# Kernel tuning notes

Hardware: AMD Instinct MI355X
Metric: run time of the kernel (lower is better)

## Reference

```python
import jax, jax.numpy as jnp
import numpy as np

KS = (7, 7)
ST = (3, 3)
PD = (3, 3)
DIM = 512
HID = 1960  # 40 * 49, divisible by kernel_shape


def _patch_flat_idx(out_h, out_w):
    kh, kw = KS; sh, sw = ST; ph, pw = PD
    oh = (out_h + 2 * ph - kh) // sh + 1
    ow = (out_w + 2 * pw - kw) // sw + 1
    Wp = out_w + 2 * pw
    iy = jnp.arange(kh)[:, None, None, None] + (jnp.arange(oh) * sh)[None, None, :, None]
    ix = jnp.arange(kw)[None, :, None, None] + (jnp.arange(ow) * sw)[None, None, None, :]
    # (kh, kw, oh, ow) flat index into padded image
    return (iy * Wp + ix), oh, ow


def fold(patches, out_h, out_w):
    # patches: (B, C*kh*kw, L) -> (B, C, out_h, out_w), overlap-add like F.fold
    kh, kw = KS; ph, pw = PD
    idx, oh, ow = _patch_flat_idx(out_h, out_w)
    B, CK, L = patches.shape
    C = CK // (kh * kw)
    Hp, Wp = out_h + 2 * ph, out_w + 2 * pw
    p = patches.reshape(B, C, kh, kw, oh, ow)
    out = jnp.zeros((B, C, Hp * Wp), patches.dtype)
    out = out.at[:, :, idx.reshape(-1)].add(p.reshape(B, C, -1))
    return out.reshape(B, C, Hp, Wp)[:, :, ph:ph + out_h, pw:pw + out_w]


def unfold(img, out_h, out_w):
    # img: (B, C, H, W) -> (B, C*kh*kw, L), like F.unfold
    kh, kw = KS; ph, pw = PD
    idx, oh, ow = _patch_flat_idx(out_h, out_w)
    B, C = img.shape[:2]
    imgp = jnp.pad(img, ((0, 0), (0, 0), (ph, ph), (pw, pw)))
    flat = imgp.reshape(B, C, -1)
    g = flat[:, :, idx.reshape(-1)].reshape(B, C, kh, kw, oh, ow)
    return g.reshape(B, C * kh * kw, oh * ow)


def setup_inputs() -> dict:
    key = jax.random.key(0)
    k1, k2, k3, k4, k5 = jax.random.split(key, 5)
    x = jax.random.normal(k1, (2, 5760, DIM), dtype=jnp.float32)
    W1 = jax.random.normal(k2, (HID, DIM), dtype=jnp.float32) * 0.02
    b1 = jax.random.normal(k3, (HID,), dtype=jnp.float32) * 0.02
    W2 = jax.random.normal(k4, (DIM, HID), dtype=jnp.float32) * 0.02
    b2 = jax.random.normal(k5, (DIM,), dtype=jnp.float32) * 0.02
    return {"x": x, "W1": W1, "b1": b1, "W2": W2, "b2": b2, "out_h": 60, "out_w": 108}


def reference(x, W1, b1, W2, b2, out_h, out_w):
    kh, kw = KS; sh, sw = ST; ph, pw = PD
    oh = (out_h + 2 * ph - kh) // sh + 1
    ow = (out_w + 2 * pw - kw) // sw + 1
    n_vecs = oh * ow
    h = jnp.einsum('bnd,hd->bnh', x, W1) + b1          # (b, n, HID)
    b_, n, c = h.shape
    p = h.reshape(-1, n_vecs, c).transpose(0, 2, 1)     # (B', c, L)
    folded = fold(p, out_h, out_w)                      # (B', c//49, H, W)
    ones = jnp.ones((p.shape[0], kh * kw, n_vecs), h.dtype)
    norm = fold(ones, out_h, out_w)                     # (B', 1, H, W)
    y = unfold(folded / norm, out_h, out_w)             # (B', c, L)
    y = y.transpose(0, 2, 1).reshape(b_, n, c)
    out = jnp.einsum('bnh,dh->bnd', jax.nn.gelu(y, approximate=False), W2) + b2
    return out
```

## Files before the change

### kernel.cpp

```cpp
#include <hip/hip_runtime.h>
#include <cmath>

#define M_ROWS   11520
#define DIM      512
#define HID      1960
#define HIDP     2048
#define KP2      1984
#define OH       20
#define OW       36
#define LVEC     720
#define NCH      40
#define BPRIME   16
#define HP       66
#define WP       114

typedef unsigned short u16;
typedef __bf16 bf16x8 __attribute__((ext_vector_type(8)));
typedef float  f32x4  __attribute__((ext_vector_type(4)));

__device__ __forceinline__ u16 f2bf(float f) {
    unsigned u = __float_as_uint(f);
    u += 0x7fffu + ((u >> 16) & 1u);
    return (u16)(u >> 16);
}
__device__ __forceinline__ float bf2f(u16 h) {
    return __uint_as_float(((unsigned)h) << 16);
}

__device__ __forceinline__ void gload_lds16(const void* g, void* l) {
    __builtin_amdgcn_global_load_lds(
        (const __attribute__((address_space(1))) void*)g,
        (__attribute__((address_space(3))) void*)l, 16, 0, 0);
}

__global__ __launch_bounds__(256) void cvt_x(const float* __restrict__ src,
                                             u16* __restrict__ dst, int n) {
    int i = (blockIdx.x * 256 + threadIdx.x) * 4;
    if (i < n) {
        float4 v = *(const float4*)(src + i);
        ushort4 o;
        o.x = f2bf(v.x); o.y = f2bf(v.y); o.z = f2bf(v.z); o.w = f2bf(v.w);
        *(ushort4*)(dst + i) = o;
    }
}

__global__ __launch_bounds__(256) void cvt_w1(const float* __restrict__ src,
                                              u16* __restrict__ dst) {
    int i = (blockIdx.x * 256 + threadIdx.x) * 4;
    ushort4 o;
    if (i < HID * DIM) {
        float4 v = *(const float4*)(src + i);
        o.x = f2bf(v.x); o.y = f2bf(v.y); o.z = f2bf(v.z); o.w = f2bf(v.w);
    } else {
        o.x = o.y = o.z = o.w = 0;
    }
    *(ushort4*)(dst + i) = o;
}

__global__ __launch_bounds__(256) void cvt_w2(const float* __restrict__ src,
                                              u16* __restrict__ dst) {
    int i = (blockIdx.x * 256 + threadIdx.x) * 4;
    int d = i / HIDP, c = i % HIDP;
    ushort4 o;
    if (c < HID) {
        float4 v = *(const float4*)(src + d * HID + c);
        o.x = f2bf(v.x); o.y = f2bf(v.y); o.z = f2bf(v.z); o.w = f2bf(v.w);
    } else {
        o.x = o.y = o.z = o.w = 0;
    }
    *(ushort4*)(dst + i) = o;
}

template <int OUT_BF16, int BN>
__global__ __launch_bounds__(256) void gemm_bt(const u16* __restrict__ A,
                                               const u16* __restrict__ B,
                                               const float* __restrict__ bias,
                                               int biasN, void* __restrict__ Cout,
                                               int N, int K, int ldk) {
    constexpr int WN = BN / 2;
    constexpr int NU = WN / 16;

    __shared__ u16 sA[128 * 64];
    __shared__ u16 sB[BN * 64];

    const int tid  = threadIdx.x;
    const int ntn  = N / BN;
    const int NB   = gridDim.x;
    const int v    = (blockIdx.x & 7) * (NB >> 3) + (blockIdx.x >> 3);
    const int bm   = v / ntn;
    const int bn   = v - bm * ntn;
    const int lane = tid & 63;
    const int wv   = tid >> 6;
    const int wm   = (wv >> 1) * 64;
    const int wn   = (wv & 1) * WN;
    const int r    = lane & 15;
    const int quad = lane >> 4;

    const size_t Arow0 = (size_t)bm * 128 * ldk;
    const size_t Brow0 = (size_t)bn * BN * ldk;

    f32x4 acc[4][NU] = {};

    for (int kt = 0; kt < K; kt += 64) {
        __syncthreads();
#pragma unroll
        for (int i = 0; i < 4; i++) {
            int e   = i * 256 + tid;
            int row = e >> 3;
            int cp  = e & 7;
            int cg  = cp ^ (row & 7);
            gload_lds16(A + Arow0 + (size_t)row * ldk + kt + cg * 8, (char*)sA + e * 16);
        }
#pragma unroll
        for (int i = 0; i < (BN * 8) / 256; i++) {
            int e   = i * 256 + tid;
            int row = e >> 3;
            int cp  = e & 7;
            int cg  = cp ^ (row & 7);
            gload_lds16(B + Brow0 + (size_t)row * ldk + kt + cg * 8, (char*)sB + e * 16);
        }
        __syncthreads();
#pragma unroll
        for (int kk = 0; kk < 2; kk++) {
            bf16x8 af[4], bg[NU];
#pragma unroll
            for (int t = 0; t < 4; t++) {
                int row = wm + t * 16 + r;
                int c   = (kk * 4 + quad) ^ (row & 7);
                af[t] = *(const bf16x8*)(sA + row * 64 + c * 8);
            }
#pragma unroll
            for (int u = 0; u < NU; u++) {
                int row = wn + u * 16 + r;
                int c   = (kk * 4 + quad) ^ (row & 7);
                bg[u] = *(const bf16x8*)(sB + row * 64 + c * 8);
            }
#pragma unroll
            for (int t = 0; t < 4; t++)
#pragma unroll
                for (int u = 0; u < NU; u++)
                    acc[t][u] = __builtin_amdgcn_mfma_f32_16x16x32_bf16(
                        af[t], bg[u], acc[t][u], 0, 0, 0);
        }
    }

    const int gm0 = bm * 128 + wm;
    const int gn0 = bn * BN + wn;
#pragma unroll
    for (int u = 0; u < NU; u++) {
        int gn = gn0 + u * 16 + r;
        float bv = (gn < biasN) ? bias[gn] : 0.0f;
#pragma unroll
        for (int t = 0; t < 4; t++) {
            int gm = gm0 + t * 16 + quad * 4;
#pragma unroll
            for (int q = 0; q < 4; q++) {
                float v2 = acc[t][u][q] + bv;
                if (OUT_BF16)
                    ((u16*)Cout)[(size_t)(gm + q) * N + gn] = f2bf(v2);
                else
                    ((float*)Cout)[(size_t)(gm + q) * N + gn] = v2;
            }
        }
    }
}

__global__ __launch_bounds__(256) void midA_fold(const u16* __restrict__ hg,
                                                 u16* __restrict__ G) {
    __shared__ u16 sh[7 * OW * 49];

    const int b  = blockIdx.x;
    const int bp = b / (NCH * 4);
    const int rr = b - bp * (NCH * 4);
    const int ch = rr >> 2;
    const int s  = rr & 3;
    const int lo    = (s == 0) ? 0 : (5 * s - 2);
    const int nload = (s == 0) ? 5 : 7;
    const int row0  = 15 * s;
    const int nrows = (s == 3) ? 21 : 15;
    const int n0 = bp * LVEC;
    const int c0 = ch * 49;
    const int tid = threadIdx.x;

    for (int i = tid; i < nload * OW * 49; i += 256) {
        int l = i / 49, k = i - l * 49;
        sh[i] = hg[(size_t)(n0 + lo * OW + l) * HIDP + c0 + k];
    }
    __syncthreads();

    const int px = tid & 127;
    const int rg = tid >> 7;
    if (px >= WP) return;

    const bool pxin = (px >= 3) && (px <= 110);
    const int kx0 = px % 3;
    int  ct[3];
    bool vx[3];
    int  cx = 0;
#pragma unroll
    for (int dx = 0; dx < 3; dx++) {
        int kx = kx0 + 3 * dx, rx = px - kx;
        bool ok = pxin && (kx <= 6) && (rx >= 0) && (rx <= 105);
        vx[dx] = ok;
        ct[dx] = ok ? ((rx / 3) * 49 + kx) : 0;
        cx += ok ? 1 : 0;
    }
    const float fcx = (cx == 3) ? (1.0f / 3.0f) : ((cx == 2) ? 0.5f : 1.0f);

    u16* Gb = G + (size_t)(bp * NCH + ch) * (HP * WP);
    for (int ri = rg; ri < nrows; ri += 2) {
        int py = row0 + ri;
        float val = 0.0f;
        if (pxin && py >= 3 && py <= 62) {
            int ky0 = py % 3;
            float sum = 0.0f;
            int cy = 0;
#pragma unroll
            for (int dy = 0; dy < 3; dy++) {
                int ky = ky0 + 3 * dy, ry = py - ky;
                if (ky <= 6 && ry >= 0 && ry <= 57) {
                    int rt = (ry / 3 - lo) * (OW * 49) + ky * 7;
                    cy++;
                    float v0 = bf2f(sh[rt + ct[0]]);
                    float v1 = bf2f(sh[rt + ct[1]]);
                    float v2 = bf2f(sh[rt + ct[2]]);
                    sum += vx[0] ? v0 : 0.0f;
                    sum += vx[1] ? v1 : 0.0f;
                    sum += vx[2] ? v2 : 0.0f;
                }
            }
            float fcy = (cy == 3) ? (1.0f / 3.0f) : ((cy == 2) ? 0.5f : 1.0f);
            float m = sum * fcx * fcy;
            val = 0.5f * m * (1.0f + erff(m * 0.70710678118654752f));
        }
        Gb[py * WP + px] = f2bf(val);
    }
}

__global__ __launch_bounds__(256) void midB_unfold(const u16* __restrict__ G,
                                                   u16* __restrict__ hg) {
    __shared__ u16 sG[34 * WP];

    const int b  = blockIdx.x;
    const int bp = b / (NCH * 2);
    const int rr = b - bp * (NCH * 2);
    const int ch = rr >> 1;
    const int s  = rr & 1;
    const int o0 = s * 10;
    const int n0 = bp * LVEC + o0 * OW;
    const int c0 = ch * 49;
    const int tid = threadIdx.x;

    const u16* Gb = G + (size_t)(bp * NCH + ch) * (HP * WP) + 3 * o0 * WP;
    for (int p = tid; p < 34 * WP; p += 256) sG[p] = Gb[p];
    __syncthreads();

    for (int i = tid; i < 10 * OW * 49; i += 256) {
        int l = i / 49, k = i - l * 49;
        int ky = k / 7, kx = k - ky * 7;
        int oy = l / OW, ox = l - oy * OW;
        hg[(size_t)(n0 + l) * HIDP + c0 + k] = sG[(3 * oy + ky) * WP + kx + 3 * ox];
    }
}

extern "C" void kernel_launch(void* const* d_in, const int* in_sizes, int n_in,
                              void* d_out, int out_size, void* d_ws, size_t ws_size,
                              hipStream_t stream) {
    (void)in_sizes; (void)n_in; (void)out_size; (void)ws_size;
    const float* x  = (const float*)d_in[0];
    const float* W1 = (const float*)d_in[1];
    const float* b1 = (const float*)d_in[2];
    const float* W2 = (const float*)d_in[3];
    const float* b2 = (const float*)d_in[4];
    float* out = (float*)d_out;

    char* ws = (char*)d_ws;
    u16* xb  = (u16*)(ws);
    u16* W1b = (u16*)(ws + 11796480);
    u16* W2b = (u16*)(ws + 11796480 + 2097152);
    u16* hg  = (u16*)(ws + 11796480 + 2097152 + 2097152);
    u16* G   = xb;

    cvt_x <<<(M_ROWS * DIM) / (256 * 4), 256, 0, stream>>>(x, xb, M_ROWS * DIM);
    cvt_w1<<<(HIDP * DIM) / (256 * 4), 256, 0, stream>>>(W1, W1b);
    cvt_w2<<<(DIM * HIDP) / (256 * 4), 256, 0, stream>>>(W2, W2b);

    gemm_bt<1, 128><<<(M_ROWS / 128) * (HIDP / 128), 256, 0, stream>>>(
        xb, W1b, b1, HID, (void*)hg, HIDP, DIM, DIM);

    midA_fold<<<BPRIME * NCH * 4, 256, 0, stream>>>(hg, G);
    midB_unfold<<<BPRIME * NCH * 2, 256, 0, stream>>>(G, hg);

    gemm_bt<0, 64><<<(M_ROWS / 128) * (DIM / 64), 256, 0, stream>>>(
        hg, W2b, b2, DIM, (void*)out, DIM, KP2, HIDP);
}
```

Measured before the change: 209.5 us.

## Merge conversion kernels and run GEMMs with 512-thread blocks of 8 waves

Folds the three fp32-to-bf16 conversion kernels into one launch that picks its source by block index, saving two kernel launches. The GEMM now uses 512 threads, so each of 8 waves computes a 32-row slice instead of 64 rows with 4 waves. This halves per-wave accumulators and raises the number of waves sharing each LDS tile, trading register pressure for more latency hiding. Each wave now issues fewer MFMAs per LDS fragment load, which raises LDS traffic relative to compute.

```diff
diff --git a/kernel.cpp b/kernel.cpp
--- a/kernel.cpp
+++ b/kernel.cpp
@@ -33,52 +33,53 @@
         (__attribute__((address_space(3))) void*)l, 16, 0, 0);
 }
 
-__global__ __launch_bounds__(256) void cvt_x(const float* __restrict__ src,
-                                             u16* __restrict__ dst, int n) {
-    int i = (blockIdx.x * 256 + threadIdx.x) * 4;
-    if (i < n) {
-        float4 v = *(const float4*)(src + i);
-        ushort4 o;
+#define CVT_XB   5760
+#define CVT_W1B  1024
+__global__ __launch_bounds__(256) void cvt_all(const float* __restrict__ x,
+                                               const float* __restrict__ W1,
+                                               const float* __restrict__ W2,
+                                               u16* __restrict__ xb,
+                                               u16* __restrict__ W1b,
+                                               u16* __restrict__ W2b) {
+    const int b = blockIdx.x;
+    const int tid = threadIdx.x;
+    ushort4 o;
+    if (b < CVT_XB) {
+        int i = (b * 256 + tid) * 4;
+        float4 v = *(const float4*)(x + i);
         o.x = f2bf(v.x); o.y = f2bf(v.y); o.z = f2bf(v.z); o.w = f2bf(v.w);
-        *(ushort4*)(dst + i) = o;
-    }
-}
-
-__global__ __launch_bounds__(256) void cvt_w1(const float* __restrict__ src,
-                                              u16* __restrict__ dst) {
-    int i = (blockIdx.x * 256 + threadIdx.x) * 4;
-    ushort4 o;
-    if (i < HID * DIM) {
-        float4 v = *(const float4*)(src + i);
-        o.x = f2bf(v.x); o.y = f2bf(v.y); o.z = f2bf(v.z); o.w = f2bf(v.w);
+        *(ushort4*)(xb + i) = o;
+    } else if (b < CVT_XB + CVT_W1B) {
+        int i = ((b - CVT_XB) * 256 + tid) * 4;
+        if (i < HID * DIM) {
+            float4 v = *(const float4*)(W1 + i);
+            o.x = f2bf(v.x); o.y = f2bf(v.y); o.z = f2bf(v.z); o.w = f2bf(v.w);
+        } else {
+            o.x = o.y = o.z = o.w = 0;
+        }
+        *(ushort4*)(W1b + i) = o;
     } else {
-        o.x = o.y = o.z = o.w = 0;
-    }
-    *(ushort4*)(dst + i) = o;
-}
-
-__global__ __launch_bounds__(256) void cvt_w2(const float* __restrict__ src,
-                                              u16* __restrict__ dst) {
-    int i = (blockIdx.x * 256 + threadIdx.x) * 4;
-    int d = i / HIDP, c = i % HIDP;
-    ushort4 o;
-    if (c < HID) {
-        float4 v = *(const float4*)(src + d * HID + c);
-        o.x = f2bf(v.x); o.y = f2bf(v.y); o.z = f2bf(v.z); o.w = f2bf(v.w);
-    } else {
-        o.x = o.y = o.z = o.w = 0;
-    }
-    *(ushort4*)(dst + i) = o;
+        int i = ((b - CVT_XB - CVT_W1B) * 256 + tid) * 4;
+        int d = i / HIDP, c = i - d * HIDP;
+        if (c < HID) {
+            float4 v = *(const float4*)(W2 + (size_t)d * HID + c);
+            o.x = f2bf(v.x); o.y = f2bf(v.y); o.z = f2bf(v.z); o.w = f2bf(v.w);
+        } else {
+            o.x = o.y = o.z = o.w = 0;
+        }
+        *(ushort4*)(W2b + i) = o;
+    }
 }
 
 template <int OUT_BF16, int BN>
-__global__ __launch_bounds__(256) void gemm_bt(const u16* __restrict__ A,
+__global__ __launch_bounds__(512) void gemm_bt(const u16* __restrict__ A,
                                                const u16* __restrict__ B,
                                                const float* __restrict__ bias,
                                                int biasN, void* __restrict__ Cout,
                                                int N, int K, int ldk) {
     constexpr int WN = BN / 2;
     constexpr int NU = WN / 16;
+    constexpr int BCH = BN * 8;
 
     __shared__ u16 sA[128 * 64];
     __shared__ u16 sB[BN * 64];
@@ -91,7 +92,7 @@
     const int bn   = v - bm * ntn;
     const int lane = tid & 63;
     const int wv   = tid >> 6;
-    const int wm   = (wv >> 1) * 64;
+    const int wm   = (wv >> 1) * 32;
     const int wn   = (wv & 1) * WN;
     const int r    = lane & 15;
     const int quad = lane >> 4;
@@ -99,21 +100,21 @@
     const size_t Arow0 = (size_t)bm * 128 * ldk;
     const size_t Brow0 = (size_t)bn * BN * ldk;
 
-    f32x4 acc[4][NU] = {};
+    f32x4 acc[2][NU] = {};
 
     for (int kt = 0; kt < K; kt += 64) {
         __syncthreads();
 #pragma unroll
-        for (int i = 0; i < 4; i++) {
-            int e   = i * 256 + tid;
+        for (int i = 0; i < 2; i++) {
+            int e   = i * 512 + tid;
             int row = e >> 3;
             int cp  = e & 7;
             int cg  = cp ^ (row & 7);
             gload_lds16(A + Arow0 + (size_t)row * ldk + kt + cg * 8, (char*)sA + e * 16);
         }
 #pragma unroll
-        for (int i = 0; i < (BN * 8) / 256; i++) {
-            int e   = i * 256 + tid;
+        for (int i = 0; i < BCH / 512; i++) {
+            int e   = i * 512 + tid;
             int row = e >> 3;
             int cp  = e & 7;
             int cg  = cp ^ (row & 7);
@@ -122,9 +123,9 @@
         __syncthreads();
 #pragma unroll
         for (int kk = 0; kk < 2; kk++) {
-            bf16x8 af[4], bg[NU];
-#pragma unroll
-            for (int t = 0; t < 4; t++) {
+            bf16x8 af[2], bg[NU];
+#pragma unroll
+            for (int t = 0; t < 2; t++) {
                 int row = wm + t * 16 + r;
                 int c   = (kk * 4 + quad) ^ (row & 7);
                 af[t] = *(const bf16x8*)(sA + row * 64 + c * 8);
@@ -136,7 +137,7 @@
                 bg[u] = *(const bf16x8*)(sB + row * 64 + c * 8);
             }
 #pragma unroll
-            for (int t = 0; t < 4; t++)
+            for (int t = 0; t < 2; t++)
 #pragma unroll
                 for (int u = 0; u < NU; u++)
                     acc[t][u] = __builtin_amdgcn_mfma_f32_16x16x32_bf16(
@@ -151,7 +152,7 @@
         int gn = gn0 + u * 16 + r;
         float bv = (gn < biasN) ? bias[gn] : 0.0f;
 #pragma unroll
-        for (int t = 0; t < 4; t++) {
+        for (int t = 0; t < 2; t++) {
             int gm = gm0 + t * 16 + quad * 4;
 #pragma unroll
             for (int q = 0; q < 4; q++) {
@@ -281,16 +282,14 @@
     u16* hg  = (u16*)(ws + 11796480 + 2097152 + 2097152);
     u16* G   = xb;
 
-    cvt_x <<<(M_ROWS * DIM) / (256 * 4), 256, 0, stream>>>(x, xb, M_ROWS * DIM);
-    cvt_w1<<<(HIDP * DIM) / (256 * 4), 256, 0, stream>>>(W1, W1b);
-    cvt_w2<<<(DIM * HIDP) / (256 * 4), 256, 0, stream>>>(W2, W2b);
-
-    gemm_bt<1, 128><<<(M_ROWS / 128) * (HIDP / 128), 256, 0, stream>>>(
+    cvt_all<<<CVT_XB + 2 * CVT_W1B, 256, 0, stream>>>(x, W1, W2, xb, W1b, W2b);
+
+    gemm_bt<1, 128><<<(M_ROWS / 128) * (HIDP / 128), 512, 0, stream>>>(
         xb, W1b, b1, HID, (void*)hg, HIDP, DIM, DIM);
 
     midA_fold<<<BPRIME * NCH * 4, 256, 0, stream>>>(hg, G);
     midB_unfold<<<BPRIME * NCH * 2, 256, 0, stream>>>(G, hg);
 
-    gemm_bt<0, 64><<<(M_ROWS / 128) * (DIM / 64), 256, 0, stream>>>(
+    gemm_bt<0, 64><<<(M_ROWS / 128) * (DIM / 64), 512, 0, stream>>>(
         hg, W2b, b2, DIM, (void*)out, DIM, KP2, HIDP);
 }
```

New measurement: 204.3 us. -2.4%, faster.
